# Kernel optimization log

Measured on AMD Instinct MI355X. Metric: run time of the kernel, lower is better.

Reference implementation:

```python
import jax, jax.numpy as jnp
import numpy as np

B, C, H, W = 16, 4, 512, 512


def setup_inputs() -> dict:
    key = jax.random.key(0)
    k_in, k_tg, k_mask = jax.random.split(key, 3)
    inp = jax.random.normal(k_in, (B, C, H, W), dtype=jnp.float32)
    tgt_vals = jax.random.normal(k_tg, (B, C, H, W), dtype=jnp.float32)
    mask = jax.random.randint(k_mask, (B, 1, H, W), 0, 2).astype(jnp.float32)
    target = jnp.concatenate([tgt_vals, mask], axis=1)  # [B, C+1, H, W]
    return {"input": inp, "target": target}


def reference(input, target):
    # mask = target[b, -1]; masked_select broadcasts mask over the C channels,
    # MSELoss means over the C*count selected elements; batches with empty
    # masks contribute 0; each batch contribution is divided by B.
    mask = (target[:, -1] == 1).astype(input.dtype)            # [B, H, W]
    diff2 = jnp.square(input - target[:, :-1])                 # [B, C, H, W]
    sum_b = jnp.einsum("bchw,bhw->b", diff2, mask)             # masked SSE per batch
    cnt_b = mask.sum(axis=(1, 2)) * input.shape[1]             # C * #masked pixels
    per_b = jnp.where(cnt_b > 0, sum_b / jnp.maximum(cnt_b, 1.0), 0.0)
    return per_b.sum() / input.shape[0]
```

## Files before the change

kernel.cpp:

```cpp
#include <hip/hip_runtime.h>


#define BATCH 16
#define CHAN 4
#define HWPIX (512 * 512)
#define BLOCKS_PER_BATCH 64
#define THREADS 512
#define TOTAL_BLOCKS (BATCH * BLOCKS_PER_BATCH)

__global__ __launch_bounds__(THREADS) void masked_mse_partial(
    const float* __restrict__ input,
    const float* __restrict__ target,
    float* __restrict__ ws) {
    const int b   = blockIdx.x / BLOCKS_PER_BATCH;
    const int blk = blockIdx.x % BLOCKS_PER_BATCH;

    const int groups           = HWPIX / 4;
    const int groups_per_block = groups / BLOCKS_PER_BATCH;

    const float* inb = input  + (size_t)b * CHAN * HWPIX;
    const float* tgb = target + (size_t)b * (CHAN + 1) * HWPIX;
    const float4* mask4 = (const float4*)(tgb + (size_t)CHAN * HWPIX);

    float s = 0.f, cnt = 0.f;

    const int g_end = (blk + 1) * groups_per_block;
#pragma unroll 2
    for (int g = blk * groups_per_block + threadIdx.x; g < g_end; g += THREADS) {
        float4 m = mask4[g];
        float mx = (m.x == 1.f) ? 1.f : 0.f;
        float my = (m.y == 1.f) ? 1.f : 0.f;
        float mz = (m.z == 1.f) ? 1.f : 0.f;
        float mw = (m.w == 1.f) ? 1.f : 0.f;
        cnt += mx + my + mz + mw;
#pragma unroll
        for (int c = 0; c < CHAN; ++c) {
            float4 a = ((const float4*)(inb + (size_t)c * HWPIX))[g];
            float4 t = ((const float4*)(tgb + (size_t)c * HWPIX))[g];
            float dx = a.x - t.x, dy = a.y - t.y, dz = a.z - t.z, dw = a.w - t.w;
            s += dx * dx * mx + dy * dy * my + dz * dz * mz + dw * dw * mw;
        }
    }

#pragma unroll
    for (int off = 32; off > 0; off >>= 1) {
        s   += __shfl_down(s, off, 64);
        cnt += __shfl_down(cnt, off, 64);
    }

    __shared__ float ss[THREADS / 64];
    __shared__ float sc[THREADS / 64];
    const int lane = threadIdx.x & 63;
    const int wid  = threadIdx.x >> 6;
    if (lane == 0) { ss[wid] = s; sc[wid] = cnt; }
    __syncthreads();

    if (threadIdx.x == 0) {
        float S = 0.f, Cn = 0.f;
#pragma unroll
        for (int w = 0; w < THREADS / 64; ++w) { S += ss[w]; Cn += sc[w]; }
        atomicAdd(&ws[2 * b],     S);
        atomicAdd(&ws[2 * b + 1], Cn);
    }
}

__global__ void masked_mse_final(const float* __restrict__ ws,
                                 float* __restrict__ out) {
    if (threadIdx.x == 0 && blockIdx.x == 0) {
        float acc = 0.f;
#pragma unroll
        for (int b = 0; b < BATCH; ++b) {
            float s  = ws[2 * b];
            float cb = ws[2 * b + 1] * (float)CHAN;
            acc += (cb > 0.f) ? (s / cb) : 0.f;
        }
        out[0] = acc / (float)BATCH;
    }
}

extern "C" void kernel_launch(void* const* d_in, const int* in_sizes, int n_in,
                              void* d_out, int out_size, void* d_ws, size_t ws_size,
                              hipStream_t stream) {
    const float* input  = (const float*)d_in[0];
    const float* target = (const float*)d_in[1];
    float* out = (float*)d_out;
    float* ws  = (float*)d_ws;

    hipMemsetAsync(ws, 0, 2 * BATCH * sizeof(float), stream);

    masked_mse_partial<<<dim3(TOTAL_BLOCKS), dim3(THREADS), 0, stream>>>(
        input, target, ws);
    masked_mse_final<<<1, 64, 0, stream>>>(ws, out);
}
```

Measured before the change: 176.5 us.

## Stage per-block pixel chunks into LDS via direct global-to-LDS loads

Each block now handles a 1024-pixel chunk of one batch and uses global_load_lds (buffer-to-LDS, 16 bytes per lane) to copy all nine planes (4 input, 4 target, 1 mask) into shared memory. After a barrier, each thread computes one float4 group from LDS. The aim is to issue all loads up front, bypassing VGPRs, to get more memory-level parallelism. In exchange, the grid grows to 4096 blocks with 36KB of LDS each, which means more atomics and more per-block overhead, and the 16-byte global_load_lds width requires gfx950 support.

```diff
diff --git a/kernel.cpp b/kernel.cpp
--- a/kernel.cpp
+++ b/kernel.cpp
@@ -4,61 +4,78 @@
 #define BATCH 16
 #define CHAN 4
 #define HWPIX (512 * 512)
-#define BLOCKS_PER_BATCH 64
-#define THREADS 512
-#define TOTAL_BLOCKS (BATCH * BLOCKS_PER_BATCH)
+#define PX_PER_BLOCK 1024
+#define THREADS 256
+#define WAVES (THREADS / 64)
+#define CHUNKS_PER_BATCH (HWPIX / PX_PER_BLOCK)
+#define TOTAL_BLOCKS (BATCH * CHUNKS_PER_BATCH)
+#define PLANES (2 * CHAN + 1)
+#define SEGS (PLANES * 4)
+#define SEGS_PER_WAVE (SEGS / WAVES)
+
+typedef __attribute__((address_space(3))) float       lds_f32;
+typedef __attribute__((address_space(1))) const float g_f32c;
 
 __global__ __launch_bounds__(THREADS) void masked_mse_partial(
     const float* __restrict__ input,
     const float* __restrict__ target,
     float* __restrict__ ws) {
-    const int b   = blockIdx.x / BLOCKS_PER_BATCH;
-    const int blk = blockIdx.x % BLOCKS_PER_BATCH;
+    __shared__ float smem[PLANES * PX_PER_BLOCK];
+    __shared__ float ss[WAVES], sc[WAVES];
 
-    const int groups           = HWPIX / 4;
-    const int groups_per_block = groups / BLOCKS_PER_BATCH;
+    const int b = blockIdx.x / CHUNKS_PER_BATCH;
+    const int k = blockIdx.x % CHUNKS_PER_BATCH;
 
-    const float* inb = input  + (size_t)b * CHAN * HWPIX;
-    const float* tgb = target + (size_t)b * (CHAN + 1) * HWPIX;
-    const float4* mask4 = (const float4*)(tgb + (size_t)CHAN * HWPIX);
+    const float* inb = input  + (size_t)b * CHAN * HWPIX       + (size_t)k * PX_PER_BLOCK;
+    const float* tgb = target + (size_t)b * (CHAN + 1) * HWPIX + (size_t)k * PX_PER_BLOCK;
 
-    float s = 0.f, cnt = 0.f;
+    const int lane = threadIdx.x & 63;
+    const int w    = threadIdx.x >> 6;
 
-    const int g_end = (blk + 1) * groups_per_block;
-#pragma unroll 2
-    for (int g = blk * groups_per_block + threadIdx.x; g < g_end; g += THREADS) {
-        float4 m = mask4[g];
-        float mx = (m.x == 1.f) ? 1.f : 0.f;
-        float my = (m.y == 1.f) ? 1.f : 0.f;
-        float mz = (m.z == 1.f) ? 1.f : 0.f;
-        float mw = (m.w == 1.f) ? 1.f : 0.f;
-        cnt += mx + my + mz + mw;
 #pragma unroll
-        for (int c = 0; c < CHAN; ++c) {
-            float4 a = ((const float4*)(inb + (size_t)c * HWPIX))[g];
-            float4 t = ((const float4*)(tgb + (size_t)c * HWPIX))[g];
-            float dx = a.x - t.x, dy = a.y - t.y, dz = a.z - t.z, dw = a.w - t.w;
-            s += dx * dx * mx + dy * dy * my + dz * dz * mz + dw * dw * mw;
-        }
+    for (int j = 0; j < SEGS_PER_WAVE; ++j) {
+        const int s   = w * SEGS_PER_WAVE + j;
+        const int p   = s >> 2;
+        const int sub = s & 3;
+        const float* gp;
+        if (p < CHAN) gp = inb + (size_t)p * HWPIX + sub * 256;
+        else          gp = tgb + (size_t)(p - CHAN) * HWPIX + sub * 256;
+        __builtin_amdgcn_global_load_lds(
+            (g_f32c*)(gp + lane * 4),
+            (lds_f32*)(smem + s * 256),
+            16, 0, 0);
+    }
+
+    __syncthreads();
+
+    const int t = threadIdx.x;
+    float4 m4 = ((const float4*)(smem + 2 * CHAN * PX_PER_BLOCK))[t];
+    float mx = (m4.x == 1.f) ? 1.f : 0.f;
+    float my = (m4.y == 1.f) ? 1.f : 0.f;
+    float mz = (m4.z == 1.f) ? 1.f : 0.f;
+    float mw = (m4.w == 1.f) ? 1.f : 0.f;
+    float cnt = mx + my + mz + mw;
+    float s_acc = 0.f;
+#pragma unroll
+    for (int c = 0; c < CHAN; ++c) {
+        float4 a  = ((const float4*)(smem + c * PX_PER_BLOCK))[t];
+        float4 tt = ((const float4*)(smem + (CHAN + c) * PX_PER_BLOCK))[t];
+        float dx = a.x - tt.x, dy = a.y - tt.y, dz = a.z - tt.z, dw = a.w - tt.w;
+        s_acc += dx * dx * mx + dy * dy * my + dz * dz * mz + dw * dw * mw;
     }
 
 #pragma unroll
     for (int off = 32; off > 0; off >>= 1) {
-        s   += __shfl_down(s, off, 64);
-        cnt += __shfl_down(cnt, off, 64);
+        s_acc += __shfl_down(s_acc, off, 64);
+        cnt   += __shfl_down(cnt, off, 64);
     }
-
-    __shared__ float ss[THREADS / 64];
-    __shared__ float sc[THREADS / 64];
-    const int lane = threadIdx.x & 63;
-    const int wid  = threadIdx.x >> 6;
-    if (lane == 0) { ss[wid] = s; sc[wid] = cnt; }
+    if (lane == 0) { ss[w] = s_acc; sc[w] = cnt; }
     __syncthreads();
 
-    if (threadIdx.x == 0) {
+    if (t == 0) {
         float S = 0.f, Cn = 0.f;
 #pragma unroll
-        for (int w = 0; w < THREADS / 64; ++w) { S += ss[w]; Cn += sc[w]; }
+        for (int i = 0; i < WAVES; ++i) { S += ss[i]; Cn += sc[i]; }
         atomicAdd(&ws[2 * b],     S);
         atomicAdd(&ws[2 * b + 1], Cn);
     }
```

Result: slower. 211.7 us (+19.9%).

## Restructure masked MSE into per-chunk blocks with batched nontemporal vector loads

Applied to the files above, without the earlier changes.

Splits each batch image into fixed 4096-pixel chunks, one per 256-thread block. Each thread loads its mask vectors once, then issues several vector loads per channel before computing, using nontemporal loads to avoid cache pollution. The mask comparison is replaced by multiplying directly by the mask value. That is cheaper but assumes the mask holds only 0 or 1. The aim is more memory-level parallelism and higher streaming bandwidth.

```diff
diff --git a/kernel.cpp b/kernel.cpp
--- a/kernel.cpp
+++ b/kernel.cpp
@@ -4,41 +4,55 @@
 #define BATCH 16
 #define CHAN 4
 #define HWPIX (512 * 512)
-#define BLOCKS_PER_BATCH 64
-#define THREADS 512
-#define TOTAL_BLOCKS (BATCH * BLOCKS_PER_BATCH)
+#define CHUNK_PX 4096
+#define CPB (HWPIX / CHUNK_PX)
+#define THREADS 256
+#define TOTAL_BLOCKS (BATCH * CPB)
+#define PER (CHUNK_PX / 4 / THREADS)
+
+typedef float vf4 __attribute__((ext_vector_type(4)));
 
 __global__ __launch_bounds__(THREADS) void masked_mse_partial(
     const float* __restrict__ input,
     const float* __restrict__ target,
     float* __restrict__ ws) {
-    const int b   = blockIdx.x / BLOCKS_PER_BATCH;
-    const int blk = blockIdx.x % BLOCKS_PER_BATCH;
+    const int u = blockIdx.x;
+    const int b = u / CPB;
+    const int k = u % CPB;
 
-    const int groups           = HWPIX / 4;
-    const int groups_per_block = groups / BLOCKS_PER_BATCH;
+    const size_t chunk_off = (size_t)k * CHUNK_PX;
+    const vf4* mp = (const vf4*)(target + ((size_t)b * (CHAN + 1) + CHAN) * HWPIX
+                                        + chunk_off);
 
-    const float* inb = input  + (size_t)b * CHAN * HWPIX;
-    const float* tgb = target + (size_t)b * (CHAN + 1) * HWPIX;
-    const float4* mask4 = (const float4*)(tgb + (size_t)CHAN * HWPIX);
+    vf4 m[PER];
+#pragma unroll
+    for (int j = 0; j < PER; ++j)
+        m[j] = __builtin_nontemporal_load(&mp[threadIdx.x + j * THREADS]);
 
-    float s = 0.f, cnt = 0.f;
+    float cnt = 0.f;
+#pragma unroll
+    for (int j = 0; j < PER; ++j) cnt += m[j].x + m[j].y + m[j].z + m[j].w;
 
-    const int g_end = (blk + 1) * groups_per_block;
-#pragma unroll 2
-    for (int g = blk * groups_per_block + threadIdx.x; g < g_end; g += THREADS) {
-        float4 m = mask4[g];
-        float mx = (m.x == 1.f) ? 1.f : 0.f;
-        float my = (m.y == 1.f) ? 1.f : 0.f;
-        float mz = (m.z == 1.f) ? 1.f : 0.f;
-        float mw = (m.w == 1.f) ? 1.f : 0.f;
-        cnt += mx + my + mz + mw;
+    float s = 0.f;
+
+#pragma unroll 1
+    for (int c = 0; c < CHAN; ++c) {
+        const vf4* ip = (const vf4*)(input  + ((size_t)b * CHAN + c) * HWPIX
+                                            + chunk_off);
+        const vf4* tp = (const vf4*)(target + ((size_t)b * (CHAN + 1) + c) * HWPIX
+                                            + chunk_off);
+        vf4 a[PER], t[PER];
 #pragma unroll
-        for (int c = 0; c < CHAN; ++c) {
-            float4 a = ((const float4*)(inb + (size_t)c * HWPIX))[g];
-            float4 t = ((const float4*)(tgb + (size_t)c * HWPIX))[g];
-            float dx = a.x - t.x, dy = a.y - t.y, dz = a.z - t.z, dw = a.w - t.w;
-            s += dx * dx * mx + dy * dy * my + dz * dz * mz + dw * dw * mw;
+        for (int j = 0; j < PER; ++j)
+            a[j] = __builtin_nontemporal_load(&ip[threadIdx.x + j * THREADS]);
+#pragma unroll
+        for (int j = 0; j < PER; ++j)
+            t[j] = __builtin_nontemporal_load(&tp[threadIdx.x + j * THREADS]);
+#pragma unroll
+        for (int j = 0; j < PER; ++j) {
+            vf4 d = a[j] - t[j];
+            vf4 p = d * d * m[j];
+            s += p.x + p.y + p.z + p.w;
         }
     }
 
@@ -86,7 +100,7 @@
     float* out = (float*)d_out;
     float* ws  = (float*)d_ws;
 
-    hipMemsetAsync(ws, 0, 2 * BATCH * sizeof(float), stream);
+    (void)hipMemsetAsync(ws, 0, 2 * BATCH * sizeof(float), stream);
 
     masked_mse_partial<<<dim3(TOTAL_BLOCKS), dim3(THREADS), 0, stream>>>(
         input, target, ws);
```

Result: faster. 170.3 us (-3.5%).
